# Kernel optimization log

Hardware: AMD Instinct MI355X
Metric: run time of the kernel (lower is better)

## Reference

```python
import jax, jax.numpy as jnp
import numpy as np

TEMP = 0.5  # init temperature
EPS = 1e-12  # F.normalize eps


def setup_inputs() -> dict:
    key = jax.random.key(0)
    k1, k2 = jax.random.split(key)
    batch_embedding = jax.random.normal(k1, (4096, 256), dtype=jnp.float32)
    labels = jax.random.randint(k2, (4096,), 0, 512, dtype=jnp.int64)
    return {"batch_embedding": batch_embedding, "labels": labels}


def reference(batch_embedding, labels):
    n = labels.shape[0]
    dt = batch_embedding.dtype
    # row-normalize; cosine_similarity of normalized rows == norm @ norm.T
    nrm = jnp.linalg.norm(batch_embedding, axis=1, keepdims=True)
    norm = batch_embedding / jnp.maximum(nrm, EPS)
    sim = norm @ norm.T  # [n, n]
    mask = (labels[:, None] == labels[None, :]).astype(dt)  # same-label pairs (incl. diagonal)
    eye = jnp.eye(n, dtype=dt)
    exp_sim = jnp.exp(sim / TEMP) * (1.0 - eye)  # zero diagonal
    pos = mask * exp_sim
    neg_sum = jnp.sum(exp_sim - pos, axis=1)  # per-row negative sum
    ratio = pos / (pos + neg_sum[:, None])
    loss_mat = -jnp.log((1.0 - mask) + ratio + eye)
    nnz = jnp.count_nonzero(loss_mat).astype(dt)
    return jnp.sum(loss_mat) / nnz
```

## Files before the change

kernel.cpp:

```cpp
#include <hip/hip_runtime.h>
#include <hip/hip_bf16.h>


#define N_ROWS 4096
#define K_DIM  256

typedef __attribute__((ext_vector_type(8))) short short8;
typedef __attribute__((ext_vector_type(4))) float float4v;
typedef __attribute__((ext_vector_type(4))) float f4;

#define PK_OFF    0
#define STATS_OFF (N_ROWS * K_DIM * 2)

__global__ void normalize_kernel(const float* __restrict__ emb,
                                 short* __restrict__ pk,
                                 float* __restrict__ stats) {
    int tile = blockIdx.x, t = threadIdx.x;
    __shared__ float lds[16 * 256];
    __shared__ float sc[16];
    const f4* src = (const f4*)(emb + tile * 16 * 256);
    f4* dst4 = (f4*)lds;
    #pragma unroll
    for (int it = 0; it < 4; ++it) dst4[t + 256 * it] = src[t + 256 * it];
    __syncthreads();
    int wave = t >> 6, lane = t & 63;
    int row = wave * 4 + (lane >> 4);
    float s = 0.f;
    #pragma unroll
    for (int m = 0; m < 16; ++m) {
        float x = lds[row * 256 + (lane & 15) + 16 * m];
        s += x * x;
    }
    s += __shfl_xor(s, 1); s += __shfl_xor(s, 2);
    s += __shfl_xor(s, 4); s += __shfl_xor(s, 8);
    float scale = 1.0f / fmaxf(sqrtf(s), 1e-12f);
    if ((lane & 15) == 0) sc[row] = scale;
    __syncthreads();
    short out[16];
    #pragma unroll
    for (int u = 0; u < 16; ++u) {
        int p = t * 16 + u;
        int j = p & 7, r16 = (p >> 3) & 15, quad = (p >> 7) & 3, c = p >> 9;
        int k = quad * 8 + c * 32 + j;
        float v = lds[r16 * 256 + k] * sc[r16];
        __hip_bfloat16 b = __float2bfloat16(v);
        out[u] = *(short*)&b;
    }
    short* dst = pk + tile * 4096 + t * 16;
    *(short8*)dst = *(short8*)out;
    *(short8*)(dst + 8) = *(short8*)(out + 8);
    if (t < 80) stats[tile * 80 + t] = 0.0f;
}

__global__ __launch_bounds__(512, 4)
void negsum_kernel(const short* __restrict__ pk,
                   const int* __restrict__ labels,
                   float* __restrict__ stats) {
    __shared__ short bs[8 * 4096];
    __shared__ int   labS[128];
    int t = threadIdx.x;
    int w = t >> 6, lane = t & 63;
    int row16 = lane & 15, quad = lane >> 4;
    int J = blockIdx.x & 31;
    int igroup = blockIdx.x >> 5;

    {
        const short8* src = (const short8*)(pk + J * 32768);
        short8* dst = (short8*)bs;
        #pragma unroll
        for (int it = 0; it < 8; ++it)
            dst[t + it * 512] = src[t + it * 512];
        if (t < 128) labS[t] = labels[J * 128 + t];
    }
    __syncthreads();

    short8 af[2][8];
    int istrip0 = igroup * 16 + w * 2;
    #pragma unroll
    for (int s = 0; s < 2; ++s) {
        const short* ap = pk + ((istrip0 + s) << 12) + lane * 8;
        #pragma unroll
        for (int c = 0; c < 8; ++c)
            af[s][c] = *(const short8*)(ap + (c << 9));
    }
    int irow[2][4], labi[2][4];
    #pragma unroll
    for (int s = 0; s < 2; ++s)
        #pragma unroll
        for (int r = 0; r < 4; ++r) {
            irow[s][r] = (istrip0 + s) * 16 + quad * 4 + r;
            labi[s][r] = labels[irow[s][r]];
        }

    float nacc[2][4] = {{0,0,0,0},{0,0,0,0}};

    for (int jt = 0; jt < 8; ++jt) {
        const short* bp = bs + (jt << 12) + lane * 8;
        float4v acc[2] = {{0.f,0.f,0.f,0.f},{0.f,0.f,0.f,0.f}};
        #pragma unroll
        for (int c = 0; c < 8; ++c) {
            short8 b = *(const short8*)(bp + (c << 9));
            acc[0] = __builtin_amdgcn_mfma_f32_16x16x32_bf16(af[0][c], b, acc[0], 0, 0, 0);
            acc[1] = __builtin_amdgcn_mfma_f32_16x16x32_bf16(af[1][c], b, acc[1], 0, 0, 0);
        }
        int j    = J * 128 + jt * 16 + row16;
        int labj = labS[jt * 16 + row16];
        #pragma unroll
        for (int s = 0; s < 2; ++s) {
            #pragma unroll
            for (int r = 0; r < 4; ++r) {
                float t2 = 2.0f * acc[s][r];
                float e  = __expf(t2);
                bool same = (labj == labi[s][r]);
                nacc[s][r] += same ? 0.0f : e;
                bool p = same && (j != irow[s][r]);
                if (__any(p)) {
                    if (p) {
                        atomicAdd(&stats[1 * N_ROWS + irow[s][r]], e);
                        atomicAdd(&stats[2 * N_ROWS + irow[s][r]], e * e);
                        atomicAdd(&stats[3 * N_ROWS + irow[s][r]], t2);
                        atomicAdd(&stats[4 * N_ROWS + irow[s][r]], 1.0f);
                    }
                }
            }
        }
    }

    #pragma unroll
    for (int s = 0; s < 2; ++s)
        #pragma unroll
        for (int r = 0; r < 4; ++r) {
            float v = nacc[s][r];
            v += __shfl_xor(v, 1); v += __shfl_xor(v, 2);
            v += __shfl_xor(v, 4); v += __shfl_xor(v, 8);
            if (row16 == 0) atomicAdd(&stats[irow[s][r]], v);
        }
}

__global__ void finalize_kernel(const float* __restrict__ stats,
                                float* __restrict__ out) {
    const float* neg   = stats;
    const float* pexp  = stats + N_ROWS;
    const float* pexp2 = stats + 2 * N_ROWS;
    const float* pt2   = stats + 3 * N_ROWS;
    const float* pcnt  = stats + 4 * N_ROWS;
    float lsum = 0.f, csum = 0.f;
    for (int i = threadIdx.x; i < N_ROWS; i += 256) {
        float c = pcnt[i];
        if (c > 0.f) {
            float n = neg[i];
            float invn = 1.0f / n;
            lsum += c * logf(n) + pexp[i] * invn
                    - 0.5f * pexp2[i] * invn * invn - pt2[i];
            csum += c;
        }
    }
    #pragma unroll
    for (int off = 32; off > 0; off >>= 1) {
        lsum += __shfl_down(lsum, off, 64);
        csum += __shfl_down(csum, off, 64);
    }
    __shared__ float sl[4], sc2[4];
    int wave = threadIdx.x >> 6, lane = threadIdx.x & 63;
    if (lane == 0) { sl[wave] = lsum; sc2[wave] = csum; }
    __syncthreads();
    if (threadIdx.x == 0)
        out[0] = (sl[0] + sl[1] + sl[2] + sl[3]) / (sc2[0] + sc2[1] + sc2[2] + sc2[3]);
}

extern "C" void kernel_launch(void* const* d_in, const int* in_sizes, int n_in,
                              void* d_out, int out_size, void* d_ws, size_t ws_size,
                              hipStream_t stream) {
    const float* emb    = (const float*)d_in[0];
    const int*   labels = (const int*)d_in[1];
    float* out = (float*)d_out;
    char*  ws  = (char*)d_ws;

    short* pk    = (short*)(ws + PK_OFF);
    float* stats = (float*)(ws + STATS_OFF);

    normalize_kernel<<<N_ROWS / 16, 256, 0, stream>>>(emb, pk, stats);
    negsum_kernel<<<512, 512, 0, stream>>>(pk, labels, stats);
    finalize_kernel<<<1, 256, 0, stream>>>(stats, out);
}
```

Measured before the change: 94.43 us.

## Replace per-element atomics with register accumulation and per-column-block partial buffers

Positive-pair statistics are now accumulated branch-free in registers with a mask multiply instead of four global atomicAdds per matching element. Each column block writes its per-row partial sums to a dedicated slot, so the negative-sum atomics also disappear. A new 16-block row-reduction kernel sums the 32 partials per row and computes the loss terms, and a tiny division kernel produces the final output. This trades atomic contention for more registers, a larger workspace and an extra kernel launch.

```diff
diff --git a/kernel.cpp b/kernel.cpp
--- a/kernel.cpp
+++ b/kernel.cpp
@@ -10,11 +10,13 @@
 typedef __attribute__((ext_vector_type(4))) float f4;
 
 #define PK_OFF    0
-#define STATS_OFF (N_ROWS * K_DIM * 2)
+#define PART_OFF  (N_ROWS * K_DIM * 2)
+#define PART_SZ   (5 * 32 * N_ROWS)
+#define ACC_OFF   (PART_OFF + PART_SZ * 4)
 
 __global__ void normalize_kernel(const float* __restrict__ emb,
                                  short* __restrict__ pk,
-                                 float* __restrict__ stats) {
+                                 float* __restrict__ acc) {
     int tile = blockIdx.x, t = threadIdx.x;
     __shared__ float lds[16 * 256];
     __shared__ float sc[16];
@@ -49,13 +51,13 @@
     short* dst = pk + tile * 4096 + t * 16;
     *(short8*)dst = *(short8*)out;
     *(short8*)(dst + 8) = *(short8*)(out + 8);
-    if (t < 80) stats[tile * 80 + t] = 0.0f;
+    if (tile == 0 && t < 2) acc[t] = 0.0f;
 }
 
 __global__ __launch_bounds__(512, 4)
 void negsum_kernel(const short* __restrict__ pk,
                    const int* __restrict__ labels,
-                   float* __restrict__ stats) {
+                   float* __restrict__ part) {
     __shared__ short bs[8 * 4096];
     __shared__ int   labS[128];
     int t = threadIdx.x;
@@ -93,6 +95,10 @@
         }
 
     float nacc[2][4] = {{0,0,0,0},{0,0,0,0}};
+    float pe[2][4]   = {{0,0,0,0},{0,0,0,0}};
+    float pe2[2][4]  = {{0,0,0,0},{0,0,0,0}};
+    float ptt[2][4]  = {{0,0,0,0},{0,0,0,0}};
+    float pc[2][4]   = {{0,0,0,0},{0,0,0,0}};
 
     for (int jt = 0; jt < 8; ++jt) {
         const short* bp = bs + (jt << 12) + lane * 8;
@@ -112,16 +118,13 @@
                 float t2 = 2.0f * acc[s][r];
                 float e  = __expf(t2);
                 bool same = (labj == labi[s][r]);
+                bool p    = same && (j != irow[s][r]);
+                float m   = p ? 1.0f : 0.0f;
                 nacc[s][r] += same ? 0.0f : e;
-                bool p = same && (j != irow[s][r]);
-                if (__any(p)) {
-                    if (p) {
-                        atomicAdd(&stats[1 * N_ROWS + irow[s][r]], e);
-                        atomicAdd(&stats[2 * N_ROWS + irow[s][r]], e * e);
-                        atomicAdd(&stats[3 * N_ROWS + irow[s][r]], t2);
-                        atomicAdd(&stats[4 * N_ROWS + irow[s][r]], 1.0f);
-                    }
-                }
+                pe[s][r]   = fmaf(m, e,      pe[s][r]);
+                pe2[s][r]  = fmaf(m, e * e,  pe2[s][r]);
+                ptt[s][r]  = fmaf(m, t2,     ptt[s][r]);
+                pc[s][r]  += m;
             }
         }
     }
@@ -130,42 +133,59 @@
     for (int s = 0; s < 2; ++s)
         #pragma unroll
         for (int r = 0; r < 4; ++r) {
-            float v = nacc[s][r];
-            v += __shfl_xor(v, 1); v += __shfl_xor(v, 2);
-            v += __shfl_xor(v, 4); v += __shfl_xor(v, 8);
-            if (row16 == 0) atomicAdd(&stats[irow[s][r]], v);
-        }
-}
-
-__global__ void finalize_kernel(const float* __restrict__ stats,
-                                float* __restrict__ out) {
-    const float* neg   = stats;
-    const float* pexp  = stats + N_ROWS;
-    const float* pexp2 = stats + 2 * N_ROWS;
-    const float* pt2   = stats + 3 * N_ROWS;
-    const float* pcnt  = stats + 4 * N_ROWS;
-    float lsum = 0.f, csum = 0.f;
-    for (int i = threadIdx.x; i < N_ROWS; i += 256) {
-        float c = pcnt[i];
-        if (c > 0.f) {
-            float n = neg[i];
-            float invn = 1.0f / n;
-            lsum += c * logf(n) + pexp[i] * invn
-                    - 0.5f * pexp2[i] * invn * invn - pt2[i];
-            csum += c;
-        }
+            float v0 = nacc[s][r], v1 = pe[s][r], v2 = pe2[s][r];
+            float v3 = ptt[s][r],  v4 = pc[s][r];
+            #pragma unroll
+            for (int m = 1; m < 16; m <<= 1) {
+                v0 += __shfl_xor(v0, m); v1 += __shfl_xor(v1, m);
+                v2 += __shfl_xor(v2, m); v3 += __shfl_xor(v3, m);
+                v4 += __shfl_xor(v4, m);
+            }
+            if (row16 == 0) {
+                int idx = J * N_ROWS + irow[s][r];
+                part[0 * 32 * N_ROWS + idx] = v0;
+                part[1 * 32 * N_ROWS + idx] = v1;
+                part[2 * 32 * N_ROWS + idx] = v2;
+                part[3 * 32 * N_ROWS + idx] = v3;
+                part[4 * 32 * N_ROWS + idx] = v4;
+            }
+        }
+}
+
+__global__ void rowreduce_kernel(const float* __restrict__ part,
+                                 float* __restrict__ acc) {
+    int i = blockIdx.x * 256 + threadIdx.x;
+    float n = 0.f, e1 = 0.f, e2 = 0.f, tt = 0.f, c = 0.f;
+    for (int J = 0; J < 32; ++J) {
+        int idx = J * N_ROWS + i;
+        n  += part[0 * 32 * N_ROWS + idx];
+        e1 += part[1 * 32 * N_ROWS + idx];
+        e2 += part[2 * 32 * N_ROWS + idx];
+        tt += part[3 * 32 * N_ROWS + idx];
+        c  += part[4 * 32 * N_ROWS + idx];
+    }
+    float lsum = 0.f;
+    if (c > 0.f) {
+        float invn = 1.0f / n;
+        lsum = c * logf(n) + e1 * invn - 0.5f * e2 * invn * invn - tt;
     }
     #pragma unroll
     for (int off = 32; off > 0; off >>= 1) {
         lsum += __shfl_down(lsum, off, 64);
-        csum += __shfl_down(csum, off, 64);
+        c    += __shfl_down(c,    off, 64);
     }
     __shared__ float sl[4], sc2[4];
     int wave = threadIdx.x >> 6, lane = threadIdx.x & 63;
-    if (lane == 0) { sl[wave] = lsum; sc2[wave] = csum; }
-    __syncthreads();
-    if (threadIdx.x == 0)
-        out[0] = (sl[0] + sl[1] + sl[2] + sl[3]) / (sc2[0] + sc2[1] + sc2[2] + sc2[3]);
+    if (lane == 0) { sl[wave] = lsum; sc2[wave] = c; }
+    __syncthreads();
+    if (threadIdx.x == 0) {
+        atomicAdd(&acc[0], sl[0] + sl[1] + sl[2] + sl[3]);
+        atomicAdd(&acc[1], sc2[0] + sc2[1] + sc2[2] + sc2[3]);
+    }
+}
+
+__global__ void div_kernel(const float* __restrict__ acc, float* __restrict__ out) {
+    if (threadIdx.x == 0) out[0] = acc[0] / acc[1];
 }
 
 extern "C" void kernel_launch(void* const* d_in, const int* in_sizes, int n_in,
@@ -176,10 +196,12 @@
     float* out = (float*)d_out;
     char*  ws  = (char*)d_ws;
 
-    short* pk    = (short*)(ws + PK_OFF);
-    float* stats = (float*)(ws + STATS_OFF);
-
-    normalize_kernel<<<N_ROWS / 16, 256, 0, stream>>>(emb, pk, stats);
-    negsum_kernel<<<512, 512, 0, stream>>>(pk, labels, stats);
-    finalize_kernel<<<1, 256, 0, stream>>>(stats, out);
-}
+    short* pk   = (short*)(ws + PK_OFF);
+    float* part = (float*)(ws + PART_OFF);
+    float* acc  = (float*)(ws + ACC_OFF);
+
+    normalize_kernel<<<N_ROWS / 16, 256, 0, stream>>>(emb, pk, acc);
+    negsum_kernel<<<512, 512, 0, stream>>>(pk, labels, part);
+    rowreduce_kernel<<<16, 256, 0, stream>>>(part, acc);
+    div_kernel<<<1, 64, 0, stream>>>(acc, out);
+}
```

Measured after the change: 83.16 us. 1.14x faster.
